# Kernel optimization log

Measured on AMD Instinct MI355X. Metric: run time of the kernel, lower is better.

The kernel has to match this reference:

```python
import jax, jax.numpy as jnp
import numpy as np
import math

B, S, E = 2, 2048, 1024
H = 16
D = E // H  # head dim = 64


def setup_inputs() -> dict:
    key = jax.random.key(0)
    ks = jax.random.split(key, 9)
    s = 1.0 / math.sqrt(E)
    return {
        "x": jax.random.normal(ks[0], (B, S, E), dtype=jnp.float32),
        "Wq": jax.random.uniform(ks[1], (E, E), jnp.float32, -s, s),
        "bq": jnp.zeros((E,), jnp.float32),
        "Wk": jax.random.uniform(ks[2], (E, E), jnp.float32, -s, s),
        "bk": jnp.zeros((E,), jnp.float32),
        "Wv": jax.random.uniform(ks[3], (E, E), jnp.float32, -s, s),
        "bv": jnp.zeros((E,), jnp.float32),
        "Wo": jax.random.uniform(ks[4], (E, E), jnp.float32, -s, s),
        "bo": jnp.zeros((E,), jnp.float32),
    }


def reference(x, Wq, bq, Wk, bk, Wv, bv, Wo, bo):
    b, s, e = x.shape
    q = x @ Wq + bq  # [B,S,E]
    k = x @ Wk + bk
    v = x @ Wv + bv
    # [B,S,E] -> [B,H,S,D]
    q = q.reshape(b, s, H, D).transpose(0, 2, 1, 3)
    k = k.reshape(b, s, H, D).transpose(0, 2, 1, 3)
    v = v.reshape(b, s, H, D).transpose(0, 2, 1, 3)
    scores = jnp.einsum('bhqd,bhkd->bhqk', q, k) / jnp.sqrt(jnp.float32(D))
    causal = jnp.tril(jnp.ones((s, s), dtype=bool))  # keep lower triangle
    scores = jnp.where(causal, scores, -jnp.inf)
    attn = jax.nn.softmax(scores, axis=-1)
    # dropout is identity in eval mode
    out = jnp.einsum('bhqk,bhkd->bhqd', attn, v)
    out = out.transpose(0, 2, 1, 3).reshape(b, s, e)
    return out @ Wo + bo
```

## Files before the change

kernel.cpp:

```cpp
#include <hip/hip_runtime.h>
#include <hip/hip_bf16.h>
#include <math.h>

#define B_ 2
#define S_ 2048
#define E_ 1024
#define H_ 16
#define D_ 64
#define M_ (B_*S_)

typedef __attribute__((ext_vector_type(8))) short short8v;
typedef __attribute__((ext_vector_type(4))) float floatx4;

__device__ __forceinline__ short f2bf(float f) {
    union { float f; unsigned u; } x; x.f = f;
    unsigned r = (x.u + 0x7fffu + ((x.u >> 16) & 1u)) >> 16;
    return (short)r;
}

__device__ __forceinline__ unsigned pk_bf16(float a, float b) {
    union { float f; unsigned u; } x, y;
    x.f = a; y.f = b;
    return __builtin_amdgcn_perm(y.u + 0x8000u, x.u + 0x8000u, 0x07060302u);
}

__device__ __forceinline__ float fast_exp2(float x) {
#if __has_builtin(__builtin_amdgcn_exp2f)
    return __builtin_amdgcn_exp2f(x);
#else
    return __expf(x * 0.6931471805599453f);
#endif
}

__device__ __forceinline__ void gl2lds16(const void* g, void* l) {
    __builtin_amdgcn_global_load_lds(
        (const __attribute__((address_space(1))) void*)g,
        (__attribute__((address_space(3))) void*)l, 16, 0, 0);
}

__global__ __launch_bounds__(256) void convert_x(
    const float* __restrict__ x, short* __restrict__ xb)
{
    const size_t i = ((size_t)blockIdx.x*256 + threadIdx.x) * 8;
    float4 a = *(const float4*)(x + i);
    float4 b = *(const float4*)(x + i + 4);
    int4 p = { (int)pk_bf16(a.x,a.y), (int)pk_bf16(a.z,a.w),
               (int)pk_bf16(b.x,b.y), (int)pk_bf16(b.z,b.w) };
    *(int4*)(xb + i) = p;
}

__global__ __launch_bounds__(256) void transpose_w(
    const float* __restrict__ W0, const float* __restrict__ W1,
    const float* __restrict__ W2, const float* __restrict__ W3,
    short* __restrict__ T0, short* __restrict__ T1,
    short* __restrict__ T2, short* __restrict__ T3)
{
    const int z = blockIdx.z;
    const float* W = (z==0)?W0:(z==1)?W1:(z==2)?W2:W3;
    short*       T = (z==0)?T0:(z==1)?T1:(z==2)?T2:T3;
    __shared__ float tile[32][33];
    const int k0 = blockIdx.y*32, n0 = blockIdx.x*32;
    const int r = threadIdx.x >> 5, c = threadIdx.x & 31;
    #pragma unroll
    for (int i=0;i<4;i++)
        tile[r+8*i][c] = W[(size_t)(k0+r+8*i)*E_ + n0 + c];
    __syncthreads();
    #pragma unroll
    for (int i=0;i<4;i++)
        T[(size_t)(n0+r+8*i)*E_ + k0 + c] = f2bf(tile[c][r+8*i]);
}

__global__ __launch_bounds__(256) void qkv_gemm(
    const short* __restrict__ xb,
    const short* __restrict__ Wtq, const short* __restrict__ Wtk, const short* __restrict__ Wtv,
    const float* __restrict__ bq, const float* __restrict__ bk, const float* __restrict__ bv,
    short* __restrict__ Qo, short* __restrict__ Ko, short* __restrict__ Vo)
{
    const int z = blockIdx.z;
    const short* Wt = (z==0) ? Wtq : (z==1) ? Wtk : Wtv;
    const float* bb = (z==0) ? bq  : (z==1) ? bk  : bv;
    short* out      = (z==0) ? Qo  : (z==1) ? Ko  : Vo;
    const float sc  = (z==0) ? 0.18033688011112042f : 1.0f;

    __shared__ __align__(16) short As[128*32];
    __shared__ __align__(16) short Bs[128*32];

    const int t = threadIdx.x;
    const int wave = t >> 6, lane = t & 63;
    const int quad = lane >> 4, l15 = lane & 15;
    const int m0 = blockIdx.y*128, n0 = blockIdx.x*128;
    const int mq = (wave & 1)*64, nq = (wave >> 1)*64;
    const int srow = lane >> 2, scol = (lane & 3)*8;

    floatx4 acc[4][4];
    #pragma unroll
    for (int i=0;i<4;i++)
        #pragma unroll
        for (int j=0;j<4;j++) acc[i][j] = (floatx4){0.f,0.f,0.f,0.f};

    for (int k0 = 0; k0 < E_; k0 += 32) {
        #pragma unroll
        for (int p=0;p<2;p++) {
            const int rb = 16*(wave*2 + p);
            gl2lds16(xb + (size_t)(m0+rb+srow)*E_ + k0 + scol, &As[rb*32]);
            gl2lds16(Wt + (size_t)(n0+rb+srow)*E_ + k0 + scol, &Bs[rb*32]);
        }
        __syncthreads();
        short8v a[4], b[4];
        #pragma unroll
        for (int mt=0;mt<4;mt++) a[mt] = *(const short8v*)&As[(mq+mt*16+l15)*32 + quad*8];
        #pragma unroll
        for (int nt=0;nt<4;nt++) b[nt] = *(const short8v*)&Bs[(nq+nt*16+l15)*32 + quad*8];
        #pragma unroll
        for (int mt=0;mt<4;mt++)
            #pragma unroll
            for (int nt=0;nt<4;nt++)
                acc[mt][nt] = __builtin_amdgcn_mfma_f32_16x16x32_bf16(a[mt], b[nt], acc[mt][nt], 0,0,0);
        __syncthreads();
    }

    #pragma unroll
    for (int nt=0;nt<4;nt++) {
        const int n = n0 + nq + nt*16 + l15;
        const float bias = bb[n];
        const int h = n >> 6, d = n & 63;
        #pragma unroll
        for (int mt=0;mt<4;mt++) {
            #pragma unroll
            for (int r=0;r<4;r++) {
                const int m = m0 + mq + mt*16 + quad*4 + r;
                const int b2 = m >> 11, s = m & (S_-1);
                const int bh = (b2<<4) + h;
                const float v = (acc[mt][nt][r] + bias) * sc;
                if (z == 0) {
                    out[((size_t)bh*S_ + s)*D_ + d] = f2bf(v);
                } else if (z == 1) {
                    const int ts = s >> 6, kk = s & 63;
                    const int c = kk*8 + ((d>>3) ^ ((kk>>2)&7));
                    out[((size_t)bh*32 + ts)*4096 + c*8 + (d&7)] = f2bf(v);
                } else {
                    const int ts = s >> 6, sk = s & 63;
                    const int c = d*8 + ((sk>>3) ^ (d&7));
                    out[((size_t)bh*32 + ts)*4096 + c*8 + (sk&7)] = f2bf(v);
                }
            }
        }
    }
}

__global__ __launch_bounds__(256, 1) void attn_kernel(
    const short* __restrict__ Q, const short* __restrict__ K, const short* __restrict__ V,
    short* __restrict__ AO)
{
    const int bh = blockIdx.x;
    const int qb = (gridDim.y - 1 - blockIdx.y) * 128;
    const int t = threadIdx.x;
    const int wave = t >> 6, lane = t & 63;
    const int quad = lane >> 4, l15 = lane & 15;

    const short* Qp = Q + (size_t)bh * (S_*D_);
    const short* Kp = K + (size_t)bh * (S_*D_);
    const short* Vp = V + (size_t)bh * (S_*D_);

    __shared__ __align__(16) short KVs[2][8192];
    __shared__ __align__(16) short Psl[2][4][2][16*72];

    const int qA = qb + wave*16;
    const int qB = qb + 64 + wave*16;
    const short* qa = Qp + (size_t)(qA + l15)*D_ + quad*8;
    const short8v qA0 = *(const short8v*)qa, qA1 = *(const short8v*)(qa + 32);
    const short* qbp = Qp + (size_t)(qB + l15)*D_ + quad*8;
    const short8v qB0 = *(const short8v*)qbp, qB1 = *(const short8v*)(qbp + 32);

    const int qrbA = qA + quad*4;
    const int qrbB = qB + quad*4;

    floatx4 oA[4], oB[4];
    #pragma unroll
    for (int i=0;i<4;i++) { oA[i] = (floatx4){0,0,0,0}; oB[i] = (floatx4){0,0,0,0}; }
    float tsA[4] = {0,0,0,0}, tsB[4] = {0,0,0,0};

    const int L = (qb >> 6) + 2;

    const int swz = l15 & 7;

    auto stage = [&](int kt, int p) {
        const short* src = ((wave < 2) ? Kp : Vp) + (size_t)kt*4096 + (wave&1)*2048 + lane*8;
        short* dst = &KVs[p][((wave < 2) ? 0 : 4096) + (wave&1)*2048];
        #pragma unroll
        for (int c=0;c<4;c++)
            gl2lds16(src + c*512, dst + c*512);
    };
    auto qk2 = [&](const short* KL, floatx4 (&sA)[4], floatx4 (&sB)[4]) {
        #pragma unroll
        for (int h=0; h<4; h++) {
            const int rowc = (4*l15 + h)*8;
            short8v b0 = *(const short8v*)(KL + (rowc + (quad       ^ swz))*8);
            short8v b1 = *(const short8v*)(KL + (rowc + ((4 + quad) ^ swz))*8);
            sA[h] = (floatx4){0.f,0.f,0.f,0.f};
            sA[h] = __builtin_amdgcn_mfma_f32_16x16x32_bf16(qA0, b0, sA[h], 0,0,0);
            sA[h] = __builtin_amdgcn_mfma_f32_16x16x32_bf16(qA1, b1, sA[h], 0,0,0);
            sB[h] = (floatx4){0.f,0.f,0.f,0.f};
            sB[h] = __builtin_amdgcn_mfma_f32_16x16x32_bf16(qB0, b0, sB[h], 0,0,0);
            sB[h] = __builtin_amdgcn_mfma_f32_16x16x32_bf16(qB1, b1, sB[h], 0,0,0);
        }
    };
    auto soft_u = [&](floatx4 (&s)[4], float* ts, short* pw, int qrb, int k0) {
        const int kk = k0 + 4*l15;
        #pragma unroll
        for (int r=0; r<4; r++) {
            const int qr = qrb + r;
            float p[4];
            #pragma unroll
            for (int h=0; h<4; h++) {
                const float e = fast_exp2(s[h][r]);
                p[h] = (kk + h > qr) ? 0.f : e;
            }
            ts[r] += (p[0] + p[1]) + (p[2] + p[3]);
            int2 pkv = { (int)pk_bf16(p[0], p[1]), (int)pk_bf16(p[2], p[3]) };
            *(int2*)(pw + (quad*4 + r)*72 + l15*4) = pkv;
        }
    };
    short8v vr[4][2];
    auto loadv = [&](const short* VL) {
        #pragma unroll
        for (int dt=0; dt<4; dt++) {
            const int rowc = (dt*16 + l15)*8;
            vr[dt][0] = *(const short8v*)(VL + (rowc + (quad       ^ swz))*8);
            vr[dt][1] = *(const short8v*)(VL + (rowc + ((4 + quad) ^ swz))*8);
        }
    };
    auto pv = [&](const short* pw, floatx4 (&o)[4]) {
        const short8v pf0 = *(const short8v*)(pw + l15*72 + quad*8);
        const short8v pf1 = *(const short8v*)(pw + l15*72 + 32 + quad*8);
        #pragma unroll
        for (int dt=0; dt<4; dt++) {
            o[dt] = __builtin_amdgcn_mfma_f32_16x16x32_bf16(pf0, vr[dt][0], o[dt], 0,0,0);
            o[dt] = __builtin_amdgcn_mfma_f32_16x16x32_bf16(pf1, vr[dt][1], o[dt], 0,0,0);
        }
    };

    stage(0, 0);
    __syncthreads();
    stage(1, 1);
    {
        const short* KL = &KVs[0][0];
        floatx4 sA[4], sB[4];
        qk2(KL, sA, sB);
        loadv(&KVs[0][4096]);
        soft_u(sA, tsA, &Psl[0][wave][0][0], qrbA, 0);
        soft_u(sB, tsB, &Psl[0][wave][1][0], qrbB, 0);
    }

    for (int kt = 1; kt < L; kt++) {
        const int p = kt & 1;
        __syncthreads();
        if (kt + 1 < L) stage(kt + 1, p ^ 1);
        const short* KL = &KVs[p][0];
        floatx4 sA[4], sB[4];
        qk2(KL, sA, sB);
        pv(&Psl[p^1][wave][0][0], oA);
        pv(&Psl[p^1][wave][1][0], oB);
        loadv(&KVs[p][4096]);
        const int k0 = kt << 6;
        soft_u(sA, tsA, &Psl[p][wave][0][0], qrbA, k0);
        soft_u(sB, tsB, &Psl[p][wave][1][0], qrbB, k0);
    }

    pv(&Psl[1][wave][0][0], oA);
    pv(&Psl[1][wave][1][0], oB);

    float lA[4], lB[4];
    #pragma unroll
    for (int r=0; r<4; r++) {
        float a = tsA[r], b = tsB[r];
        #pragma unroll
        for (int off=1; off<16; off<<=1) {
            a += __shfl_xor(a, off);
            b += __shfl_xor(b, off);
        }
        lA[r] = a; lB[r] = b;
    }

    const int b = bh >> 4, h = bh & 15;
    #pragma unroll
    for (int dt=0; dt<4; dt++) {
        #pragma unroll
        for (int r=0; r<4; r++) {
            const int d = dt*16 + l15;
            const int sA_ = qA + quad*4 + r;
            const int sB_ = qB + quad*4 + r;
            AO[((size_t)(b*S_ + sA_)*H_ + h)*D_ + d] = f2bf(oA[dt][r] / lA[r]);
            AO[((size_t)(b*S_ + sB_)*H_ + h)*D_ + d] = f2bf(oB[dt][r] / lB[r]);
        }
    }
}

__global__ __launch_bounds__(256) void out_gemm(
    const short* __restrict__ A, const short* __restrict__ Wto,
    const float* __restrict__ bo, float* __restrict__ out)
{
    __shared__ __align__(16) short As[128*32];
    __shared__ __align__(16) short Bs[128*32];

    const int t = threadIdx.x;
    const int wave = t >> 6, lane = t & 63;
    const int quad = lane >> 4, l15 = lane & 15;
    const int m0 = blockIdx.y*128, n0 = blockIdx.x*128;
    const int mq = (wave & 1)*64, nq = (wave >> 1)*64;
    const int srow = lane >> 2, scol = (lane & 3)*8;

    floatx4 acc[4][4];
    #pragma unroll
    for (int i=0;i<4;i++)
        #pragma unroll
        for (int j=0;j<4;j++) acc[i][j] = (floatx4){0.f,0.f,0.f,0.f};

    for (int k0 = 0; k0 < E_; k0 += 32) {
        #pragma unroll
        for (int p=0;p<2;p++) {
            const int rb = 16*(wave*2 + p);
            gl2lds16(A   + (size_t)(m0+rb+srow)*E_ + k0 + scol, &As[rb*32]);
            gl2lds16(Wto + (size_t)(n0+rb+srow)*E_ + k0 + scol, &Bs[rb*32]);
        }
        __syncthreads();
        short8v a[4], b[4];
        #pragma unroll
        for (int mt=0;mt<4;mt++) a[mt] = *(const short8v*)&As[(mq+mt*16+l15)*32 + quad*8];
        #pragma unroll
        for (int nt=0;nt<4;nt++) b[nt] = *(const short8v*)&Bs[(nq+nt*16+l15)*32 + quad*8];
        #pragma unroll
        for (int mt=0;mt<4;mt++)
            #pragma unroll
            for (int nt=0;nt<4;nt++)
                acc[mt][nt] = __builtin_amdgcn_mfma_f32_16x16x32_bf16(a[mt], b[nt], acc[mt][nt], 0,0,0);
        __syncthreads();
    }

    #pragma unroll
    for (int nt=0;nt<4;nt++) {
        const int n = n0 + nq + nt*16 + l15;
        const float bias = bo[n];
        #pragma unroll
        for (int mt=0;mt<4;mt++) {
            #pragma unroll
            for (int r=0;r<4;r++) {
                const int m = m0 + mq + mt*16 + quad*4 + r;
                out[(size_t)m*E_ + n] = acc[mt][nt][r] + bias;
            }
        }
    }
}

extern "C" void kernel_launch(void* const* d_in, const int* in_sizes, int n_in,
                              void* d_out, int out_size, void* d_ws, size_t ws_size,
                              hipStream_t stream)
{
    const float* x  = (const float*)d_in[0];
    const float* Wq = (const float*)d_in[1];
    const float* bq = (const float*)d_in[2];
    const float* Wk = (const float*)d_in[3];
    const float* bk = (const float*)d_in[4];
    const float* Wv = (const float*)d_in[5];
    const float* bv = (const float*)d_in[6];
    const float* Wo = (const float*)d_in[7];
    const float* bo = (const float*)d_in[8];

    short* xb  = (short*)d_ws;
    short* Tq  = xb  + (size_t)M_ * E_;
    short* Tk  = Tq  + (size_t)E_ * E_;
    short* Tv  = Tk  + (size_t)E_ * E_;
    short* To  = Tv  + (size_t)E_ * E_;
    short* Qw  = To  + (size_t)E_ * E_;
    short* Kw  = Qw  + (size_t)M_ * E_;
    short* Vw  = Kw  + (size_t)M_ * E_;
    short* AOw = Vw  + (size_t)M_ * E_;

    dim3 blk(256);
    convert_x<<<dim3((M_*E_)/(256*8)), blk, 0, stream>>>(x, xb);
    transpose_w<<<dim3(E_/32, E_/32, 4), blk, 0, stream>>>(Wq, Wk, Wv, Wo, Tq, Tk, Tv, To);
    qkv_gemm<<<dim3(E_/128, M_/128, 3), blk, 0, stream>>>(xb, Tq, Tk, Tv, bq, bk, bv, Qw, Kw, Vw);
    attn_kernel<<<dim3(B_*H_, S_/128), blk, 0, stream>>>(Qw, Kw, Vw, AOw);
    out_gemm<<<dim3(E_/128, M_/128), blk, 0, stream>>>(AOw, To, bo, (float*)d_out);
}
```

Before: 206.1 us.

## Deepen GEMM K-tiles to 64 with swizzled LDS and M-fastest block order

Both projection GEMMs now stage 64-wide K slices into LDS with an XOR swizzle, so each barrier pair covers twice the MFMA work and LDS bank conflicts drop. The QKV GEMM treats the three transposed weights as one contiguous 3072-row matrix, relying on Tq/Tk/Tv being adjacent in the workspace, and uses a 1D grid with M varying fastest so consecutive blocks share weight tiles in L2. The output GEMM uses 128x64 tiles to launch 512 blocks instead of 256, which fills more CUs. In exchange each block uses twice the LDS, and the smaller output tiles raise operand reload traffic.

```diff
diff --git a/kernel.cpp b/kernel.cpp
--- a/kernel.cpp
+++ b/kernel.cpp
@@ -38,6 +38,10 @@
         (__attribute__((address_space(3))) void*)l, 16, 0, 0);
 }
 
+__device__ __forceinline__ int swz_off(int row, int cg) {
+    return row*64 + (((cg ^ (row & 7)) & 7) << 3);
+}
+
 __global__ __launch_bounds__(256) void convert_x(
     const float* __restrict__ x, short* __restrict__ xb)
 {
@@ -71,26 +75,27 @@
 }
 
 __global__ __launch_bounds__(256) void qkv_gemm(
-    const short* __restrict__ xb,
-    const short* __restrict__ Wtq, const short* __restrict__ Wtk, const short* __restrict__ Wtv,
+    const short* __restrict__ xb, const short* __restrict__ Wt,
     const float* __restrict__ bq, const float* __restrict__ bk, const float* __restrict__ bv,
     short* __restrict__ Qo, short* __restrict__ Ko, short* __restrict__ Vo)
 {
-    const int z = blockIdx.z;
-    const short* Wt = (z==0) ? Wtq : (z==1) ? Wtk : Wtv;
-    const float* bb = (z==0) ? bq  : (z==1) ? bk  : bv;
-    short* out      = (z==0) ? Qo  : (z==1) ? Ko  : Vo;
-    const float sc  = (z==0) ? 0.18033688011112042f : 1.0f;
-
-    __shared__ __align__(16) short As[128*32];
-    __shared__ __align__(16) short Bs[128*32];
+    __shared__ __align__(16) short As[128*64];
+    __shared__ __align__(16) short Bs[128*64];
 
     const int t = threadIdx.x;
     const int wave = t >> 6, lane = t & 63;
     const int quad = lane >> 4, l15 = lane & 15;
-    const int m0 = blockIdx.y*128, n0 = blockIdx.x*128;
+    const int lin = blockIdx.x;
+    const int m0  = (lin & 31) * 128;
+    const int nf0 = (lin >> 5) * 128;
+    const int z   = nf0 >> 10;
+    const float* bb = (z==0) ? bq : (z==1) ? bk : bv;
+    short* out      = (z==0) ? Qo : (z==1) ? Ko : Vo;
+    const float sc  = (z==0) ? 0.18033688011112042f : 1.0f;
+
     const int mq = (wave & 1)*64, nq = (wave >> 1)*64;
-    const int srow = lane >> 2, scol = (lane & 3)*8;
+    const int sr8 = lane >> 3;
+    const int scs = ((lane & 7) ^ sr8) * 8;
 
     floatx4 acc[4][4];
     #pragma unroll
@@ -98,32 +103,36 @@
         #pragma unroll
         for (int j=0;j<4;j++) acc[i][j] = (floatx4){0.f,0.f,0.f,0.f};
 
-    for (int k0 = 0; k0 < E_; k0 += 32) {
-        #pragma unroll
-        for (int p=0;p<2;p++) {
-            const int rb = 16*(wave*2 + p);
-            gl2lds16(xb + (size_t)(m0+rb+srow)*E_ + k0 + scol, &As[rb*32]);
-            gl2lds16(Wt + (size_t)(n0+rb+srow)*E_ + k0 + scol, &Bs[rb*32]);
+    for (int k0 = 0; k0 < E_; k0 += 64) {
+        #pragma unroll
+        for (int c=0;c<4;c++) {
+            const int rb = wave*32 + c*8;
+            gl2lds16(xb + (size_t)(m0 +rb+sr8)*E_ + k0 + scs, &As[rb*64]);
+            gl2lds16(Wt + (size_t)(nf0+rb+sr8)*E_ + k0 + scs, &Bs[rb*64]);
         }
         __syncthreads();
-        short8v a[4], b[4];
-        #pragma unroll
-        for (int mt=0;mt<4;mt++) a[mt] = *(const short8v*)&As[(mq+mt*16+l15)*32 + quad*8];
-        #pragma unroll
-        for (int nt=0;nt<4;nt++) b[nt] = *(const short8v*)&Bs[(nq+nt*16+l15)*32 + quad*8];
-        #pragma unroll
-        for (int mt=0;mt<4;mt++)
-            #pragma unroll
-            for (int nt=0;nt<4;nt++)
-                acc[mt][nt] = __builtin_amdgcn_mfma_f32_16x16x32_bf16(a[mt], b[nt], acc[mt][nt], 0,0,0);
+        #pragma unroll
+        for (int ks=0; ks<2; ks++) {
+            const int cg = quad + ks*4;
+            short8v a[4], b[4];
+            #pragma unroll
+            for (int mt=0;mt<4;mt++) a[mt] = *(const short8v*)&As[swz_off(mq+mt*16+l15, cg)];
+            #pragma unroll
+            for (int nt=0;nt<4;nt++) b[nt] = *(const short8v*)&Bs[swz_off(nq+nt*16+l15, cg)];
+            #pragma unroll
+            for (int mt=0;mt<4;mt++)
+                #pragma unroll
+                for (int nt=0;nt<4;nt++)
+                    acc[mt][nt] = __builtin_amdgcn_mfma_f32_16x16x32_bf16(a[mt], b[nt], acc[mt][nt], 0,0,0);
+        }
         __syncthreads();
     }
 
     #pragma unroll
     for (int nt=0;nt<4;nt++) {
-        const int n = n0 + nq + nt*16 + l15;
-        const float bias = bb[n];
-        const int h = n >> 6, d = n & 63;
+        const int nw = (nf0 & 1023) + nq + nt*16 + l15;
+        const float bias = bb[nw];
+        const int h = nw >> 6, d = nw & 63;
         #pragma unroll
         for (int mt=0;mt<4;mt++) {
             #pragma unroll
@@ -181,7 +190,6 @@
     float tsA[4] = {0,0,0,0}, tsB[4] = {0,0,0,0};
 
     const int L = (qb >> 6) + 2;
-
     const int swz = l15 & 7;
 
     auto stage = [&](int kt, int p) {
@@ -244,9 +252,8 @@
     __syncthreads();
     stage(1, 1);
     {
-        const short* KL = &KVs[0][0];
         floatx4 sA[4], sB[4];
-        qk2(KL, sA, sB);
+        qk2(&KVs[0][0], sA, sB);
         loadv(&KVs[0][4096]);
         soft_u(sA, tsA, &Psl[0][wave][0][0], qrbA, 0);
         soft_u(sB, tsB, &Psl[0][wave][1][0], qrbB, 0);
@@ -256,9 +263,8 @@
         const int p = kt & 1;
         __syncthreads();
         if (kt + 1 < L) stage(kt + 1, p ^ 1);
-        const short* KL = &KVs[p][0];
         floatx4 sA[4], sB[4];
-        qk2(KL, sA, sB);
+        qk2(&KVs[p][0], sA, sB);
         pv(&Psl[p^1][wave][0][0], oA);
         pv(&Psl[p^1][wave][1][0], oB);
         loadv(&KVs[p][4096]);
@@ -300,52 +306,62 @@
     const short* __restrict__ A, const short* __restrict__ Wto,
     const float* __restrict__ bo, float* __restrict__ out)
 {
-    __shared__ __align__(16) short As[128*32];
-    __shared__ __align__(16) short Bs[128*32];
+    __shared__ __align__(16) short As[128*64];
+    __shared__ __align__(16) short Bs[64*64];
 
     const int t = threadIdx.x;
     const int wave = t >> 6, lane = t & 63;
     const int quad = lane >> 4, l15 = lane & 15;
-    const int m0 = blockIdx.y*128, n0 = blockIdx.x*128;
-    const int mq = (wave & 1)*64, nq = (wave >> 1)*64;
-    const int srow = lane >> 2, scol = (lane & 3)*8;
-
-    floatx4 acc[4][4];
-    #pragma unroll
-    for (int i=0;i<4;i++)
+    const int lin = blockIdx.x;
+    const int m0 = (lin & 31) * 128;
+    const int n0 = (lin >> 5) * 64;
+    const int sr8 = lane >> 3;
+    const int scs = ((lane & 7) ^ sr8) * 8;
+
+    floatx4 acc[2][4];
+    #pragma unroll
+    for (int i=0;i<2;i++)
         #pragma unroll
         for (int j=0;j<4;j++) acc[i][j] = (floatx4){0.f,0.f,0.f,0.f};
 
-    for (int k0 = 0; k0 < E_; k0 += 32) {
-        #pragma unroll
-        for (int p=0;p<2;p++) {
-            const int rb = 16*(wave*2 + p);
-            gl2lds16(A   + (size_t)(m0+rb+srow)*E_ + k0 + scol, &As[rb*32]);
-            gl2lds16(Wto + (size_t)(n0+rb+srow)*E_ + k0 + scol, &Bs[rb*32]);
+    for (int k0 = 0; k0 < E_; k0 += 64) {
+        #pragma unroll
+        for (int c=0;c<4;c++) {
+            const int rb = wave*32 + c*8;
+            gl2lds16(A + (size_t)(m0+rb+sr8)*E_ + k0 + scs, &As[rb*64]);
+        }
+        #pragma unroll
+        for (int c=0;c<2;c++) {
+            const int rb = wave*16 + c*8;
+            gl2lds16(Wto + (size_t)(n0+rb+sr8)*E_ + k0 + scs, &Bs[rb*64]);
         }
         __syncthreads();
-        short8v a[4], b[4];
-        #pragma unroll
-        for (int mt=0;mt<4;mt++) a[mt] = *(const short8v*)&As[(mq+mt*16+l15)*32 + quad*8];
-        #pragma unroll
-        for (int nt=0;nt<4;nt++) b[nt] = *(const short8v*)&Bs[(nq+nt*16+l15)*32 + quad*8];
-        #pragma unroll
-        for (int mt=0;mt<4;mt++)
-            #pragma unroll
-            for (int nt=0;nt<4;nt++)
-                acc[mt][nt] = __builtin_amdgcn_mfma_f32_16x16x32_bf16(a[mt], b[nt], acc[mt][nt], 0,0,0);
+        #pragma unroll
+        for (int ks=0; ks<2; ks++) {
+            const int cg = quad + ks*4;
+            short8v a[2], b[4];
+            #pragma unroll
+            for (int mt=0;mt<2;mt++) a[mt] = *(const short8v*)&As[swz_off(wave*32+mt*16+l15, cg)];
+            #pragma unroll
+            for (int nt=0;nt<4;nt++) b[nt] = *(const short8v*)&Bs[swz_off(nt*16+l15, cg)];
+            #pragma unroll
+            for (int mt=0;mt<2;mt++)
+                #pragma unroll
+                for (int nt=0;nt<4;nt++)
+                    acc[mt][nt] = __builtin_amdgcn_mfma_f32_16x16x32_bf16(a[mt], b[nt], acc[mt][nt], 0,0,0);
+        }
         __syncthreads();
     }
 
     #pragma unroll
     for (int nt=0;nt<4;nt++) {
-        const int n = n0 + nq + nt*16 + l15;
+        const int n = n0 + nt*16 + l15;
         const float bias = bo[n];
         #pragma unroll
-        for (int mt=0;mt<4;mt++) {
+        for (int mt=0;mt<2;mt++) {
             #pragma unroll
             for (int r=0;r<4;r++) {
-                const int m = m0 + mq + mt*16 + quad*4 + r;
+                const int m = m0 + wave*32 + mt*16 + quad*4 + r;
                 out[(size_t)m*E_ + n] = acc[mt][nt][r] + bias;
             }
         }
@@ -379,7 +395,7 @@
     dim3 blk(256);
     convert_x<<<dim3((M_*E_)/(256*8)), blk, 0, stream>>>(x, xb);
     transpose_w<<<dim3(E_/32, E_/32, 4), blk, 0, stream>>>(Wq, Wk, Wv, Wo, Tq, Tk, Tv, To);
-    qkv_gemm<<<dim3(E_/128, M_/128, 3), blk, 0, stream>>>(xb, Tq, Tk, Tv, bq, bk, bv, Qw, Kw, Vw);
+    qkv_gemm<<<dim3(768), blk, 0, stream>>>(xb, Tq, bq, bk, bv, Qw, Kw, Vw);
     attn_kernel<<<dim3(B_*H_, S_/128), blk, 0, stream>>>(Qw, Kw, Vw, AOw);
-    out_gemm<<<dim3(E_/128, M_/128), blk, 0, stream>>>(AOw, To, bo, (float*)d_out);
-}
+    out_gemm<<<dim3(512), blk, 0, stream>>>(AOw, To, bo, (float*)d_out);
+}
```

Measured after the change: 196.6 us. 1.05x faster.
